# Optimization experiments

Hardware: AMD Instinct MI355X
Metric: run time of the kernel (lower is better)

Reference implementation:

```python
import jax, jax.numpy as jnp
import numpy as np

N, E, G = 50000, 800000, 64      # nodes, edges, graphs
IN, H, C, OUT = 128, 8, 32, 10   # in_channels, heads, hidden_channels, out_channels
HC = H * C                        # concat head width = 256
NEG_SLOPE = 0.2


def setup_inputs() -> dict:
    key = jax.random.key(0)
    ks = jax.random.split(key, 16)
    p = lambda k, shape: (jax.random.normal(k, shape, dtype=jnp.float32) * 0.05)
    inp = {
        "x": jax.random.normal(ks[0], (N, IN), dtype=jnp.float32),
        "edge_index": jax.random.randint(ks[1], (2, E), 0, N, dtype=jnp.int64),
        "batch": jnp.sort(jax.random.randint(ks[2], (N,), 0, G, dtype=jnp.int64)),
        # layer 1: IN -> H*C
        "w1": p(ks[3], (IN, HC)), "as1": p(ks[4], (H, C)), "ad1": p(ks[5], (H, C)), "b1": p(ks[6], (HC,)),
        # layers 2,3: H*C -> H*C
        "w2": p(ks[7], (HC, HC)), "as2": p(ks[8], (H, C)), "ad2": p(ks[9], (H, C)), "b2": p(ks[10], (HC,)),
        "w3": p(ks[11], (HC, HC)), "as3": p(ks[12], (H, C)), "ad3": p(ks[13], (H, C)), "b3": p(ks[14], (HC,)),
        "lin_w": p(ks[15], (HC, OUT)), "lin_b": jnp.zeros((OUT,), jnp.float32),
    }
    return inp


def gat_conv(x, src, dst, W, a_src, a_dst, b):
    """PyG GATConv (concat heads, self-loops already in src/dst)."""
    h = (x @ W).reshape(N, H, C)                      # [N,H,C]
    s = jnp.einsum("nhc,hc->nh", h, a_src)            # source score
    d = jnp.einsum("nhc,hc->nh", h, a_dst)            # dest score
    e = jax.nn.leaky_relu(s[src] + d[dst], NEG_SLOPE)  # [Et,H]
    m = jax.ops.segment_max(e, dst, num_segments=N)   # per-dest max (stable softmax)
    ex = jnp.exp(e - m[dst])
    denom = jax.ops.segment_sum(ex, dst, num_segments=N)
    alpha = ex / (denom[dst] + 1e-16)                 # [Et,H]
    msg = h[src] * alpha[..., None]                   # [Et,H,C]
    out = jax.ops.segment_sum(msg, dst, num_segments=N)
    return out.reshape(N, HC) + b


def reference(x, edge_index, batch, w1, as1, ad1, b1, w2, as2, ad2, b2, w3, as3, ad3, b3, lin_w, lin_b):
    loop = jnp.arange(N, dtype=edge_index.dtype)
    src = jnp.concatenate([edge_index[0], loop])      # add self-loops
    dst = jnp.concatenate([edge_index[1], loop])
    for (W, a_s, a_d, b) in ((w1, as1, ad1, b1), (w2, as2, ad2, b2), (w3, as3, ad3, b3)):
        x = jax.nn.elu(gat_conv(x, src, dst, W, a_s, a_d, b))
        # dropout p=0.5 is a no-op in eval mode
    sums = jax.ops.segment_sum(x, batch, num_segments=G)
    cnt = jax.ops.segment_sum(jnp.ones((N, 1), x.dtype), batch, num_segments=G)
    pooled = sums / jnp.maximum(cnt, 1.0)             # global_mean_pool -> [G,HC]
    return pooled @ lin_w + lin_b                     # [G,OUT]
```

## Files before the change

### kernel.cpp

```cpp
#include <hip/hip_runtime.h>
#include <hip/hip_bf16.h>
#include <math.h>

#define HC 256
#define NH 8
#define NOUT 10
#define NGRAPH 64
#define BKT 64

typedef __bf16 bf16x8 __attribute__((ext_vector_type(8)));
typedef float f32x4 __attribute__((ext_vector_type(4)));

__device__ __forceinline__ float lrelu(float v) { return v > 0.f ? v : 0.2f * v; }

__device__ __forceinline__ ushort f2bu(float f) {
  __hip_bfloat16 b = __float2bfloat16(f);
  return __builtin_bit_cast(ushort, b);
}
__device__ __forceinline__ float bf2f(ushort u) {
  return __uint_as_float(((unsigned)u) << 16);
}
__device__ __forceinline__ void unp4(uint2 v, float& a, float& b, float& c, float& d) {
  a = __uint_as_float(v.x << 16);
  b = __uint_as_float(v.x & 0xffff0000u);
  c = __uint_as_float(v.y << 16);
  d = __uint_as_float(v.y & 0xffff0000u);
}

__device__ __forceinline__ void wpack_one(int idx, const float* __restrict__ w,
                                          ushort* __restrict__ wb) {
  int i = idx & 7;
  int lane = (idx >> 3) & 63;
  int ct = (idx >> 9) & 15;
  int ks = idx >> 13;
  int k = ks * 32 + (lane >> 4) * 8 + i;
  int col = ct * 16 + (lane & 15);
  wb[idx] = f2bu(w[(size_t)k * HC + col]);
}

__device__ __forceinline__ void wsdpack_one(int idx, const float* __restrict__ w,
                                            const float* __restrict__ as,
                                            const float* __restrict__ ad,
                                            ushort* __restrict__ wbsd) {
  int i = idx & 7;
  int lane = (idx >> 3) & 63;
  int ks = idx >> 9;
  int k = ks * 32 + (lane >> 4) * 8 + i;
  int col = lane & 15;
  int head = col & 7;
  const float* av = (col < 8) ? (as + head * 32) : (ad + head * 32);
  const float* wr = w + (size_t)k * HC + head * 32;
  float sum = 0.f;
#pragma unroll
  for (int j = 0; j < 32; ++j) sum += wr[j] * av[j];
  wbsd[idx] = f2bu(sum);
}

__global__ __launch_bounds__(256) void k_pack_all(
    const float* w1, const float* w2, const float* w3,
    const float* as1, const float* ad1, const float* as2, const float* ad2,
    const float* as3, const float* ad3,
    ushort* wb1, ushort* wb2, ushort* wb3,
    ushort* wbsd1, ushort* wbsd2, ushort* wbsd3,
    int* cnt, float* gsum, int K1, int Nn) {
  int idx = blockIdx.x * blockDim.x + threadIdx.x;
  int c0 = K1 * HC;
  int c1 = c0 + HC * HC;
  int c2 = c1 + HC * HC;
  int c3 = c2 + K1 * 16;
  int c4 = c3 + HC * 16;
  int c5 = c4 + HC * 16;
  int c6 = c5 + Nn;
  int c7 = c6 + NGRAPH * HC;
  if (idx < c0) wpack_one(idx, w1, wb1);
  else if (idx < c1) wpack_one(idx - c0, w2, wb2);
  else if (idx < c2) wpack_one(idx - c1, w3, wb3);
  else if (idx < c3) wsdpack_one(idx - c2, w1, as1, ad1, wbsd1);
  else if (idx < c4) wsdpack_one(idx - c3, w2, as2, ad2, wbsd2);
  else if (idx < c5) wsdpack_one(idx - c4, w3, as3, ad3, wbsd3);
  else if (idx < c6) cnt[idx - c5] = 0;
  else if (idx < c7) gsum[idx - c6] = 0.f;
}

__global__ void k_scatter(const int* __restrict__ src, const int* __restrict__ dst, int E,
                          int* __restrict__ cnt, int* __restrict__ csrc) {
  int e = blockIdx.x * blockDim.x + threadIdx.x;
  if (e < E) {
    int d = dst[e];
    int pos = atomicAdd(&cnt[d], 1);
    if (pos < BKT) csrc[(size_t)d * BKT + pos] = src[e];
  }
}

template <int K, bool F32IN>
__global__ __launch_bounds__(256) void k_gemm_sd(const void* __restrict__ xin,
                                                 const ushort* __restrict__ wb,
                                                 const ushort* __restrict__ wbsd,
                                                 ushort* __restrict__ h,
                                                 float* __restrict__ sbuf,
                                                 float* __restrict__ dbuf, int Nn) {
  int t = threadIdx.x;
  int wv = t >> 6;
  int lane = t & 63;
  int colb = lane & 15;
  int kid = lane >> 4;
  int r0 = blockIdx.x * 32;
  if (r0 >= Nn) return;
  constexpr int NKS = K / 32;

  f32x4 acc[2][4];
#pragma unroll
  for (int rt = 0; rt < 2; ++rt)
#pragma unroll
    for (int ct = 0; ct < 4; ++ct) acc[rt][ct] = (f32x4){0.f, 0.f, 0.f, 0.f};
  f32x4 accsd[2];
#pragma unroll
  for (int rt = 0; rt < 2; ++rt) accsd[rt] = (f32x4){0.f, 0.f, 0.f, 0.f};

  const ushort* arow_b[2];
  const float* arow_f[2];
#pragma unroll
  for (int rt = 0; rt < 2; ++rt) {
    int rr = r0 + rt * 16 + colb;
    if (rr >= Nn) rr = Nn - 1;
    arow_b[rt] = (const ushort*)xin + (size_t)rr * K + kid * 8;
    arow_f[rt] = (const float*)xin + (size_t)rr * K + kid * 8;
  }
  const ushort* bbase = wb + (size_t)(wv * 4) * 512 + (size_t)lane * 8;
  const ushort* sdbase = wbsd + (size_t)lane * 8;

#pragma unroll
  for (int ks = 0; ks < NKS; ++ks) {
    bf16x8 af[2];
#pragma unroll
    for (int rt = 0; rt < 2; ++rt) {
      if (F32IN) {
        float4 fa = *(const float4*)(arow_f[rt] + ks * 32);
        float4 fb = *(const float4*)(arow_f[rt] + ks * 32 + 4);
        uint4 packed;
        packed.x = (uint)f2bu(fa.x) | ((uint)f2bu(fa.y) << 16);
        packed.y = (uint)f2bu(fa.z) | ((uint)f2bu(fa.w) << 16);
        packed.z = (uint)f2bu(fb.x) | ((uint)f2bu(fb.y) << 16);
        packed.w = (uint)f2bu(fb.z) | ((uint)f2bu(fb.w) << 16);
        af[rt] = __builtin_bit_cast(bf16x8, packed);
      } else {
        uint4 araw = *(const uint4*)(arow_b[rt] + ks * 32);
        af[rt] = __builtin_bit_cast(bf16x8, araw);
      }
    }
    bf16x8 bf_[4];
#pragma unroll
    for (int ct = 0; ct < 4; ++ct) {
      uint4 braw = *(const uint4*)(bbase + (size_t)(ks * 16 + ct) * 512);
      bf_[ct] = __builtin_bit_cast(bf16x8, braw);
    }
#pragma unroll
    for (int rt = 0; rt < 2; ++rt)
#pragma unroll
      for (int ct = 0; ct < 4; ++ct)
        acc[rt][ct] = __builtin_amdgcn_mfma_f32_16x16x32_bf16(af[rt], bf_[ct], acc[rt][ct], 0, 0, 0);
    if (wv == 3) {
      uint4 sraw = *(const uint4*)(sdbase + (size_t)ks * 512);
      bf16x8 bsd = __builtin_bit_cast(bf16x8, sraw);
#pragma unroll
      for (int rt = 0; rt < 2; ++rt)
        accsd[rt] = __builtin_amdgcn_mfma_f32_16x16x32_bf16(af[rt], bsd, accsd[rt], 0, 0, 0);
    }
  }

#pragma unroll
  for (int rt = 0; rt < 2; ++rt) {
#pragma unroll
    for (int ct = 0; ct < 4; ++ct) {
#pragma unroll
      for (int q = 0; q < 4; ++q) {
        int row = r0 + rt * 16 + kid * 4 + q;
        if (row < Nn) h[(size_t)row * HC + wv * 64 + ct * 16 + colb] = f2bu(acc[rt][ct][q]);
      }
    }
  }

  if (wv == 3) {
#pragma unroll
    for (int rt = 0; rt < 2; ++rt) {
#pragma unroll
      for (int q = 0; q < 4; ++q) {
        int row = r0 + rt * 16 + kid * 4 + q;
        if (row < Nn) {
          if (colb < 8) sbuf[(size_t)row * NH + colb] = accsd[rt][q];
          else dbuf[(size_t)row * NH + (colb - 8)] = accsd[rt][q];
        }
      }
    }
  }
}

__global__ __launch_bounds__(256) void k_aggr(const ushort* __restrict__ h,
                                              const float* __restrict__ s,
                                              const float* __restrict__ dsc,
                                              const int* __restrict__ cnt,
                                              const int* __restrict__ csrc,
                                              const float* __restrict__ bias,
                                              ushort* __restrict__ xout, int Nn) {
  int wid = (blockIdx.x * blockDim.x + threadIdx.x) >> 6;
  int lane = threadIdx.x & 63;
  if (wid >= Nn) return;
  int n = wid;
  int l32 = lane & 31;
  int half = lane >> 5;
  int head8 = l32 >> 2;
  int es = lane >> 3;
  int hh = lane & 7;
  int ce = cnt[n];
  if (ce > BKT) ce = BKT;
  const int* bucket = csrc + (size_t)n * BKT;

  float d_hh = dsc[n * NH + hh];
  float eself_hh = __expf(lrelu(s[n * NH + hh] + d_hh));
  float den = 0.f;

  float acc0 = 0.f, acc1 = 0.f, acc2 = 0.f, acc3 = 0.f;
  float acc4 = 0.f, acc5 = 0.f, acc6 = 0.f, acc7 = 0.f;

  int src_all = (lane < ce) ? bucket[lane] : n;

  for (int b = 0; b < ce; b += 16) {
    int relA = b + es, relB = b + 8 + es;
    int sA = __shfl(src_all, relA, 64);
    int sB = __shfl(src_all, relB, 64);
    float sc0 = (relA < ce) ? __expf(lrelu(s[sA * NH + hh] + d_hh)) : 0.f;
    float sc1 = (relB < ce) ? __expf(lrelu(s[sB * NH + hh] + d_hh)) : 0.f;
    den += sc0 + sc1;
#pragma unroll
    for (int g = 0; g < 8; ++g) {
      int rel = b + 2 * g + half;
      int sg = __shfl(src_all, rel, 64);
      uint4 v = ((const uint4*)(h + (size_t)sg * HC))[l32];
      float ei = __shfl(g < 4 ? sc0 : sc1, ((2 * g + half) & 7) * 8 + head8, 64);
      float b0, b1, b2, b3, b4, b5, b6, b7;
      unp4(make_uint2(v.x, v.y), b0, b1, b2, b3);
      unp4(make_uint2(v.z, v.w), b4, b5, b6, b7);
      acc0 += ei * b0; acc1 += ei * b1; acc2 += ei * b2; acc3 += ei * b3;
      acc4 += ei * b4; acc5 += ei * b5; acc6 += ei * b6; acc7 += ei * b7;
    }
  }

  den += __shfl_xor(den, 8, 64);
  den += __shfl_xor(den, 16, 64);
  den += __shfl_xor(den, 32, 64);
  den += eself_hh;
  float den_h = __shfl(den, head8, 64);

  acc0 += __shfl_xor(acc0, 32, 64); acc1 += __shfl_xor(acc1, 32, 64);
  acc2 += __shfl_xor(acc2, 32, 64); acc3 += __shfl_xor(acc3, 32, 64);
  acc4 += __shfl_xor(acc4, 32, 64); acc5 += __shfl_xor(acc5, 32, 64);
  acc6 += __shfl_xor(acc6, 32, 64); acc7 += __shfl_xor(acc7, 32, 64);

  {
    uint4 vs = ((const uint4*)(h + (size_t)n * HC))[l32];
    float p = __shfl(eself_hh, head8, 64);
    float b0, b1, b2, b3, b4, b5, b6, b7;
    unp4(make_uint2(vs.x, vs.y), b0, b1, b2, b3);
    unp4(make_uint2(vs.z, vs.w), b4, b5, b6, b7);
    acc0 += p * b0; acc1 += p * b1; acc2 += p * b2; acc3 += p * b3;
    acc4 += p * b4; acc5 += p * b5; acc6 += p * b6; acc7 += p * b7;
  }

  float inv = 1.f / (den_h + 1e-16f);
  float4 bv0 = ((const float4*)bias)[l32 * 2];
  float4 bv1 = ((const float4*)bias)[l32 * 2 + 1];
  float o0 = acc0 * inv + bv0.x, o1 = acc1 * inv + bv0.y;
  float o2 = acc2 * inv + bv0.z, o3 = acc3 * inv + bv0.w;
  float o4 = acc4 * inv + bv1.x, o5 = acc5 * inv + bv1.y;
  float o6 = acc6 * inv + bv1.z, o7 = acc7 * inv + bv1.w;
  o0 = o0 > 0.f ? o0 : __expf(o0) - 1.f;
  o1 = o1 > 0.f ? o1 : __expf(o1) - 1.f;
  o2 = o2 > 0.f ? o2 : __expf(o2) - 1.f;
  o3 = o3 > 0.f ? o3 : __expf(o3) - 1.f;
  o4 = o4 > 0.f ? o4 : __expf(o4) - 1.f;
  o5 = o5 > 0.f ? o5 : __expf(o5) - 1.f;
  o6 = o6 > 0.f ? o6 : __expf(o6) - 1.f;
  o7 = o7 > 0.f ? o7 : __expf(o7) - 1.f;
  if (half == 0) {
    uint4 o;
    o.x = (uint)f2bu(o0) | ((uint)f2bu(o1) << 16);
    o.y = (uint)f2bu(o2) | ((uint)f2bu(o3) << 16);
    o.z = (uint)f2bu(o4) | ((uint)f2bu(o5) << 16);
    o.w = (uint)f2bu(o6) | ((uint)f2bu(o7) << 16);
    ((uint4*)(xout + (size_t)n * HC))[l32] = o;
  }
}

__global__ __launch_bounds__(256) void k_pool1(const ushort* __restrict__ x,
                                               const int* __restrict__ batch,
                                               float* __restrict__ sums, int Nn) {
  __shared__ int bg[64];
  int n0 = blockIdx.x * 64;
  if (n0 >= Nn) return;
  int t = threadIdx.x;
  int n1 = n0 + 64;
  if (n1 > Nn) n1 = Nn;
  if (t < 64 && n0 + t < Nn) bg[t] = batch[n0 + t];
  __syncthreads();
  float acc = 0.f;
  int gcur = bg[0];
  for (int n = n0; n < n1; ++n) {
    int g = bg[n - n0];
    if (g != gcur) {
      atomicAdd(&sums[gcur * HC + t], acc);
      acc = 0.f;
      gcur = g;
    }
    acc += bf2f(x[(size_t)n * HC + t]);
  }
  atomicAdd(&sums[gcur * HC + t], acc);
}

__global__ __launch_bounds__(256) void k_pool2(const float* __restrict__ sums,
                                               const int* __restrict__ batch,
                                               const float* __restrict__ lw,
                                               const float* __restrict__ lb,
                                               float* __restrict__ out, int Nn) {
  __shared__ float pooled[HC];
  int g = blockIdx.x;
  int t = threadIdx.x;
  int a = 0, b = Nn;
  while (a < b) { int mid = (a + b) >> 1; if (batch[mid] < g) a = mid + 1; else b = mid; }
  int lo = a;
  b = Nn;
  while (a < b) { int mid = (a + b) >> 1; if (batch[mid] < g + 1) a = mid + 1; else b = mid; }
  int hi = a;
  int cnt = hi - lo;
  pooled[t] = sums[g * HC + t] / (float)(cnt > 0 ? cnt : 1);
  __syncthreads();
  if (t < NOUT) {
    float acc = lb[t];
    for (int c = 0; c < HC; ++c) acc += pooled[c] * lw[c * NOUT + t];
    out[g * NOUT + t] = acc;
  }
}

extern "C" void kernel_launch(void* const* d_in, const int* in_sizes, int n_in,
                              void* d_out, int out_size, void* d_ws, size_t ws_size,
                              hipStream_t stream) {
  const float* x_in = (const float*)d_in[0];
  const int* ei     = (const int*)d_in[1];
  const int* batch  = (const int*)d_in[2];
  const float* w1 = (const float*)d_in[3];
  const float* as1 = (const float*)d_in[4];
  const float* ad1 = (const float*)d_in[5];
  const float* b1 = (const float*)d_in[6];
  const float* w2 = (const float*)d_in[7];
  const float* as2 = (const float*)d_in[8];
  const float* ad2 = (const float*)d_in[9];
  const float* b2 = (const float*)d_in[10];
  const float* w3 = (const float*)d_in[11];
  const float* as3 = (const float*)d_in[12];
  const float* ad3 = (const float*)d_in[13];
  const float* b3 = (const float*)d_in[14];
  const float* lw = (const float*)d_in[15];
  const float* lb = (const float*)d_in[16];

  int Nn = in_sizes[2];
  int E = in_sizes[1] / 2;
  const int* esrc = ei;
  const int* edst = ei + E;
  int K1 = in_sizes[0] / Nn;

  char* ws = (char*)d_ws;
  size_t off = 0;
  auto alloc = [&](size_t bytes) {
    char* p = ws + off;
    off += (bytes + 255) & ~(size_t)255;
    return p;
  };
  ushort* xbuf = (ushort*)alloc((size_t)Nn * HC * 2);
  ushort* hbuf = (ushort*)alloc((size_t)Nn * HC * 2);
  ushort* wb1 = (ushort*)alloc((size_t)K1 * HC * 2);
  ushort* wb2 = (ushort*)alloc((size_t)HC * HC * 2);
  ushort* wb3 = (ushort*)alloc((size_t)HC * HC * 2);
  ushort* wbsd1 = (ushort*)alloc((size_t)K1 * 16 * 2);
  ushort* wbsd2 = (ushort*)alloc((size_t)HC * 16 * 2);
  ushort* wbsd3 = (ushort*)alloc((size_t)HC * 16 * 2);
  float* sbuf = (float*)alloc((size_t)Nn * NH * 4);
  float* dbuf = (float*)alloc((size_t)Nn * NH * 4);
  float* gsum = (float*)alloc((size_t)NGRAPH * HC * 4);
  int* cnt  = (int*)alloc((size_t)Nn * 4);
  int* csrc = (int*)alloc((size_t)Nn * BKT * 4);

  int packTotal = K1 * HC + 2 * HC * HC + K1 * 16 + 2 * HC * 16 + Nn + NGRAPH * HC;
  k_pack_all<<<(packTotal + 255) / 256, 256, 0, stream>>>(
      w1, w2, w3, as1, ad1, as2, ad2, as3, ad3,
      wb1, wb2, wb3, wbsd1, wbsd2, wbsd3, cnt, gsum, K1, Nn);

  k_scatter<<<(E + 255) / 256, 256, 0, stream>>>(esrc, edst, E, cnt, csrc);

  const ushort* Wb[3] = {wb1, wb2, wb3};
  const ushort* Wsd[3] = {wbsd1, wbsd2, wbsd3};
  const float* Bs[3] = {b1, b2, b3};

  int gemmGrid = (Nn + 31) / 32;
  int waveGrid = ((Nn * 64) + 255) / 256;
  for (int l = 0; l < 3; ++l) {
    if (l == 0)
      k_gemm_sd<128, true><<<gemmGrid, 256, 0, stream>>>(x_in, Wb[l], Wsd[l], hbuf, sbuf, dbuf, Nn);
    else
      k_gemm_sd<256, false><<<gemmGrid, 256, 0, stream>>>(xbuf, Wb[l], Wsd[l], hbuf, sbuf, dbuf, Nn);
    k_aggr<<<waveGrid, 256, 0, stream>>>(hbuf, sbuf, dbuf, cnt, csrc, Bs[l], xbuf, Nn);
  }
  k_pool1<<<(Nn + 63) / 64, 256, 0, stream>>>(xbuf, batch, gsum, Nn);
  k_pool2<<<NGRAPH, 256, 0, stream>>>(gsum, batch, lw, lb, (float*)d_out, Nn);
}
```

Measured before the change: 379.0 us.

## Split aggregation across two waves per node, each handling four heads

The aggregation kernel now assigns two wavefronts per destination node, each covering half of the heads (128 channels). Each wave loads 256-byte half-rows per edge with four edges in flight per iteration, and reduces across quarters. This doubles the number of waves to expose more parallelism and memory-level concurrency. In exchange the per-edge score and source-index work is duplicated across both waves, and there are more shuffle reductions per node.

```diff
diff --git a/kernel.cpp b/kernel.cpp
--- a/kernel.cpp
+++ b/kernel.cpp
@@ -204,39 +204,39 @@
                                               ushort* __restrict__ xout, int Nn) {
   int wid = (blockIdx.x * blockDim.x + threadIdx.x) >> 6;
   int lane = threadIdx.x & 63;
-  if (wid >= Nn) return;
-  int n = wid;
-  int l32 = lane & 31;
-  int half = lane >> 5;
-  int head8 = l32 >> 2;
-  int es = lane >> 3;
-  int hh = lane & 7;
+  int n = wid >> 1;
+  int hs = wid & 1;
+  if (n >= Nn) return;
+  int l16 = lane & 15;
+  int quarter = lane >> 4;
+  int hdl = l16 >> 2;
+  int es = lane >> 2;
+  int hh4 = lane & 3;
   int ce = cnt[n];
   if (ce > BKT) ce = BKT;
   const int* bucket = csrc + (size_t)n * BKT;
 
-  float d_hh = dsc[n * NH + hh];
-  float eself_hh = __expf(lrelu(s[n * NH + hh] + d_hh));
+  float d_hh = dsc[n * NH + hs * 4 + hh4];
+  float eself_hh = __expf(lrelu(s[n * NH + hs * 4 + hh4] + d_hh));
   float den = 0.f;
 
   float acc0 = 0.f, acc1 = 0.f, acc2 = 0.f, acc3 = 0.f;
   float acc4 = 0.f, acc5 = 0.f, acc6 = 0.f, acc7 = 0.f;
 
   int src_all = (lane < ce) ? bucket[lane] : n;
+  const ushort* hbase = h + (size_t)hs * 128;
 
   for (int b = 0; b < ce; b += 16) {
-    int relA = b + es, relB = b + 8 + es;
-    int sA = __shfl(src_all, relA, 64);
-    int sB = __shfl(src_all, relB, 64);
-    float sc0 = (relA < ce) ? __expf(lrelu(s[sA * NH + hh] + d_hh)) : 0.f;
-    float sc1 = (relB < ce) ? __expf(lrelu(s[sB * NH + hh] + d_hh)) : 0.f;
-    den += sc0 + sc1;
-#pragma unroll
-    for (int g = 0; g < 8; ++g) {
-      int rel = b + 2 * g + half;
-      int sg = __shfl(src_all, rel, 64);
-      uint4 v = ((const uint4*)(h + (size_t)sg * HC))[l32];
-      float ei = __shfl(g < 4 ? sc0 : sc1, ((2 * g + half) & 7) * 8 + head8, 64);
+    int rel = b + es;
+    int sA = __shfl(src_all, rel, 64);
+    float sc = (rel < ce) ? __expf(lrelu(s[sA * NH + hs * 4 + hh4] + d_hh)) : 0.f;
+    den += sc;
+#pragma unroll
+    for (int g = 0; g < 4; ++g) {
+      int relg = b + 4 * g + quarter;
+      int sg = __shfl(src_all, relg, 64);
+      uint4 v = ((const uint4*)(hbase + (size_t)sg * HC))[l16];
+      float ei = __shfl(sc, relg * 4 + hdl, 64);
       float b0, b1, b2, b3, b4, b5, b6, b7;
       unp4(make_uint2(v.x, v.y), b0, b1, b2, b3);
       unp4(make_uint2(v.z, v.w), b4, b5, b6, b7);
@@ -245,20 +245,25 @@
     }
   }
 
+  den += __shfl_xor(den, 4, 64);
   den += __shfl_xor(den, 8, 64);
   den += __shfl_xor(den, 16, 64);
   den += __shfl_xor(den, 32, 64);
   den += eself_hh;
-  float den_h = __shfl(den, head8, 64);
-
+  float den_h = __shfl(den, hdl, 64);
+
+  acc0 += __shfl_xor(acc0, 16, 64); acc1 += __shfl_xor(acc1, 16, 64);
+  acc2 += __shfl_xor(acc2, 16, 64); acc3 += __shfl_xor(acc3, 16, 64);
+  acc4 += __shfl_xor(acc4, 16, 64); acc5 += __shfl_xor(acc5, 16, 64);
+  acc6 += __shfl_xor(acc6, 16, 64); acc7 += __shfl_xor(acc7, 16, 64);
   acc0 += __shfl_xor(acc0, 32, 64); acc1 += __shfl_xor(acc1, 32, 64);
   acc2 += __shfl_xor(acc2, 32, 64); acc3 += __shfl_xor(acc3, 32, 64);
   acc4 += __shfl_xor(acc4, 32, 64); acc5 += __shfl_xor(acc5, 32, 64);
   acc6 += __shfl_xor(acc6, 32, 64); acc7 += __shfl_xor(acc7, 32, 64);
 
   {
-    uint4 vs = ((const uint4*)(h + (size_t)n * HC))[l32];
-    float p = __shfl(eself_hh, head8, 64);
+    uint4 vs = ((const uint4*)(hbase + (size_t)n * HC))[l16];
+    float p = __shfl(eself_hh, hdl, 64);
     float b0, b1, b2, b3, b4, b5, b6, b7;
     unp4(make_uint2(vs.x, vs.y), b0, b1, b2, b3);
     unp4(make_uint2(vs.z, vs.w), b4, b5, b6, b7);
@@ -267,8 +272,8 @@
   }
 
   float inv = 1.f / (den_h + 1e-16f);
-  float4 bv0 = ((const float4*)bias)[l32 * 2];
-  float4 bv1 = ((const float4*)bias)[l32 * 2 + 1];
+  float4 bv0 = ((const float4*)bias)[hs * 32 + l16 * 2];
+  float4 bv1 = ((const float4*)bias)[hs * 32 + l16 * 2 + 1];
   float o0 = acc0 * inv + bv0.x, o1 = acc1 * inv + bv0.y;
   float o2 = acc2 * inv + bv0.z, o3 = acc3 * inv + bv0.w;
   float o4 = acc4 * inv + bv1.x, o5 = acc5 * inv + bv1.y;
@@ -281,13 +286,13 @@
   o5 = o5 > 0.f ? o5 : __expf(o5) - 1.f;
   o6 = o6 > 0.f ? o6 : __expf(o6) - 1.f;
   o7 = o7 > 0.f ? o7 : __expf(o7) - 1.f;
-  if (half == 0) {
+  if (quarter == 0) {
     uint4 o;
     o.x = (uint)f2bu(o0) | ((uint)f2bu(o1) << 16);
     o.y = (uint)f2bu(o2) | ((uint)f2bu(o3) << 16);
     o.z = (uint)f2bu(o4) | ((uint)f2bu(o5) << 16);
     o.w = (uint)f2bu(o6) | ((uint)f2bu(o7) << 16);
-    ((uint4*)(xout + (size_t)n * HC))[l32] = o;
+    ((uint4*)(xout + (size_t)n * HC + hs * 128))[l16] = o;
   }
 }
 
@@ -400,7 +405,7 @@
   const float* Bs[3] = {b1, b2, b3};
 
   int gemmGrid = (Nn + 31) / 32;
-  int waveGrid = ((Nn * 64) + 255) / 256;
+  int waveGrid = (int)(((size_t)Nn * 128 + 255) / 256);
   for (int l = 0; l < 3; ++l) {
     if (l == 0)
       k_gemm_sd<128, true><<<gemmGrid, 256, 0, stream>>>(x_in, Wb[l], Wsd[l], hbuf, sbuf, dbuf, Nn);
```

Result: no change. 385.9 us (+1.8%).
